# Performance work log

Hardware: AMD Instinct MI355X
Metric: run time of the kernel (lower is better)

The kernel has to match this reference:

```python
import jax, jax.numpy as jnp
import numpy as np
import math

B, S, E, H, F, V, L = 2, 2048, 1024, 16, 4096, 32000, 2
D = E // H
START = 1
EPS = 1e-6


def setup_inputs() -> dict:
    key = jax.random.key(0)
    ks = jax.random.split(key, 16)
    k_emb = 1.0 / math.sqrt(V)
    std = 0.02
    inp = {
        "tokens": jax.random.randint(ks[0], (B, S), 0, V),
        "word_embed": jax.random.normal(ks[1], (V, E), jnp.float32) * k_emb,
        "pos_embed": jax.random.normal(ks[2], (S, E), jnp.float32) * k_emb,
        "unembed_b": jnp.zeros((V,), jnp.float32),
        "kqv_w": jax.random.normal(ks[3], (L, 3 * E, E), jnp.float32) * std,
        "wo_w": jax.random.normal(ks[4], (L, E, E), jnp.float32) * std,
        "up_w": jax.random.normal(ks[5], (L, F, E), jnp.float32) * std,
        "up_b": jnp.zeros((L, F), jnp.float32),
        "down_w": jax.random.normal(ks[6], (L, E, F), jnp.float32) * std,
        "down_b": jnp.zeros((L, E), jnp.float32),
        "ln1_s": jnp.ones((L, E), jnp.float32),
        "ln1_b": jnp.zeros((L, E), jnp.float32),
        "ln2_s": jnp.ones((L, E), jnp.float32),
        "ln2_b": jnp.zeros((L, E), jnp.float32),
    }
    return inp


def _layer_norm(x, scale, bias):
    m = jnp.mean(x, axis=-1, keepdims=True)
    v = jnp.var(x, axis=-1, keepdims=True)  # biased, matches torch LayerNorm
    return (x - m) / jnp.sqrt(v + EPS) * scale + bias


def _causal_block_mask(tokens):
    # block-diagonal segments split at START tokens, plus causal triu
    is_start = tokens == START
    seg = jnp.cumsum(is_start, axis=1)  # [B,S]
    block = seg[:, :, None] != seg[:, None, :]  # [B,S,S]
    triu = jnp.triu(jnp.ones((S, S), bool), k=1)
    return triu[None, :, :] | block  # [B,S,S], True = masked


def _resetting_positions(tokens):
    is_start = tokens == START
    is_start = is_start.at[:, 0].set(True)
    pos = jnp.arange(S)
    start_pos = jnp.where(is_start, pos[None, :], 0)
    last_start = jax.lax.cummax(start_pos, axis=1)
    return pos[None, :] - last_start  # [B,S]


def reference(tokens, word_embed, pos_embed, unembed_b, kqv_w, wo_w,
              up_w, up_b, down_w, down_b, ln1_s, ln1_b, ln2_s, ln2_b):
    mask = _causal_block_mask(tokens)[:, None, :, :]  # [B,1,S,S]
    rel_pos = _resetting_positions(tokens)
    x = word_embed[tokens] + pos_embed[rel_pos]  # [B,S,E]
    scale = 1.0 / math.sqrt(D)

    for l in range(L):
        # attention
        qkv = (x @ kqv_w[l].T).reshape(B, S, 3, H, D)
        k, q, v = qkv[:, :, 0], qkv[:, :, 1], qkv[:, :, 2]  # [B,S,H,D]
        attn = jnp.einsum('bqhd,bkhd->bhqk', q, k) * scale
        attn = jnp.where(mask, -jnp.inf, attn)
        attn = jax.nn.softmax(attn, axis=-1)
        out = jnp.einsum('bhqk,bkhd->bqhd', attn, v).reshape(B, S, E)
        out = out @ wo_w[l].T
        x = _layer_norm(out + x, ln1_s[l], ln1_b[l])
        # FFN
        h = jax.nn.relu(x @ up_w[l].T + up_b[l])
        h = h @ down_w[l].T + down_b[l]
        x = _layer_norm(h + x, ln2_s[l], ln2_b[l])

    # weight-tied unembed
    logits = x @ word_embed.T + unembed_b  # [B,S,V]
    return logits
```

## Files before the change

kernel.cpp:

```cpp
#include <hip/hip_runtime.h>
#include <hip/hip_bf16.h>

#define BB 2
#define SS 2048
#define EE 1024
#define HH 16
#define DD 64
#define FF 4096
#define VV 32000
#define LL 2
#define BS (BB*SS)

#define NEG_HUGE (-3.402823466e+38f)

typedef __attribute__((ext_vector_type(4)))  float  f32x4;
typedef __attribute__((ext_vector_type(16))) float  f32x16;
typedef __attribute__((ext_vector_type(8)))  __bf16 bf16x8;
typedef __attribute__((ext_vector_type(4)))  __bf16 bf16x4;

__device__ inline bf16x8 to_bf8(float4 a, float4 b) {
  bf16x8 r;
  r[0] = (__bf16)a.x; r[1] = (__bf16)a.y; r[2] = (__bf16)a.z; r[3] = (__bf16)a.w;
  r[4] = (__bf16)b.x; r[5] = (__bf16)b.y; r[6] = (__bf16)b.z; r[7] = (__bf16)b.w;
  return r;
}

typedef const unsigned int __attribute__((address_space(1)))* gptr_t;
typedef unsigned int __attribute__((address_space(3)))* lptr_t;
__device__ inline void gload16(const void* g, void* l) {
  __builtin_amdgcn_global_load_lds((gptr_t)g, (lptr_t)l, 16, 0, 0);
}

__global__ __launch_bounds__(1024) void lastart_scan(
    const int* __restrict__ tokens, int* __restrict__ ls) {
  __shared__ int buf[SS];
  const int b = blockIdx.x, t = threadIdx.x;
#pragma unroll
  for (int j = 0; j < 2; ++j) {
    int i = t + j * 1024;
    buf[i] = (i > 0 && tokens[b*SS + i] == 1) ? i : 0;
  }
  __syncthreads();
  for (int off = 1; off < SS; off <<= 1) {
    int i0 = t, i1 = t + 1024;
    int v0 = (i0 >= off) ? max(buf[i0], buf[i0 - off]) : buf[i0];
    int v1 = (i1 >= off) ? max(buf[i1], buf[i1 - off]) : buf[i1];
    __syncthreads();
    buf[i0] = v0; buf[i1] = v1;
    __syncthreads();
  }
#pragma unroll
  for (int j = 0; j < 2; ++j) {
    int i = t + j * 1024;
    ls[b*SS + i] = buf[i];
  }
}

__global__ __launch_bounds__(256) void embed_kernel(
    const int* __restrict__ tokens, const int* __restrict__ ls,
    const float* __restrict__ we, const float* __restrict__ pe,
    float* __restrict__ x, __bf16* __restrict__ xb) {
  int row = blockIdx.x;
  int s = row & (SS - 1);
  int tok = tokens[row];
  int rp = s - ls[row];
  const float4* w4 = (const float4*)(we + (size_t)tok * EE);
  const float4* p4 = (const float4*)(pe + (size_t)rp * EE);
  float4 a = w4[threadIdx.x];
  float4 b = p4[threadIdx.x];
  float4 o; o.x = a.x + b.x; o.y = a.y + b.y; o.z = a.z + b.z; o.w = a.w + b.w;
  ((float4*)(x + (size_t)row * EE))[threadIdx.x] = o;
  bf16x4 ob4;
  ob4[0] = (__bf16)o.x; ob4[1] = (__bf16)o.y; ob4[2] = (__bf16)o.z; ob4[3] = (__bf16)o.w;
  *(bf16x4*)(xb + (size_t)row * EE + threadIdx.x * 4) = ob4;
}

__global__ __launch_bounds__(256) void cvt_bf16_kernel(
    const float* __restrict__ src, __bf16* __restrict__ dst, int n) {
  int i = (blockIdx.x * 256 + threadIdx.x) * 8;
  if (i + 8 > n) return;
  float4 a = *(const float4*)(src + i);
  float4 b = *(const float4*)(src + i + 4);
  *(bf16x8*)(dst + i) = to_bf8(a, b);
}

__device__ inline void stage_half(const __bf16* __restrict__ base,
                                  __bf16* region, int K, int kofs, int t) {
  const int col8 = (t & 3) ^ ((t >> 3) & 3);
  const int csrc = kofs + col8 * 8;
  const int wbase = (t >> 6) * 512;
#pragma unroll
  for (int p = 0; p < 2; ++p)
    gload16(base + (size_t)(p * 128 + (t >> 2)) * K + csrc, region + p * 4096 + wbase);
}

#define SWZ(row) ((c8 ^ (((row) >> 1) & 3)) * 8)

template<bool BIAS, bool RELU, bool OUTBF16>
__global__ __launch_bounds__(512, 2) void gemm_8ph(
    const __bf16* __restrict__ A, const __bf16* __restrict__ W,
    const float* __restrict__ bias, void* __restrict__ Cv,
    int N, int K, int nbx) {
  __shared__ __bf16 lds[2][2][2][8192];
  const int t = threadIdx.x, l = t & 63, w = t >> 6;
  const int nwg = gridDim.x, orig = blockIdx.x;
  const int q = nwg >> 3, r = nwg & 7, xcd = orig & 7, pos = orig >> 3;
  const int wgid = (xcd < r ? xcd*(q+1) : r*(q+1) + (xcd-r)*q) + pos;
  const int m0 = (wgid % nbx) * 256, n0 = (wgid / nbx) * 256;
  const int wm = w >> 2, wn = w & 3;
  const int fr = l & 15, c8 = l >> 4;

  const __bf16* Ab = A + (size_t)m0 * K;
  const __bf16* Wb = W + (size_t)n0 * K;

  f32x4 acc[8][4] = {};
  const int nk = K >> 6;

  stage_half(Ab, &lds[0][0][0][0], K, 0,  t);
  stage_half(Wb, &lds[0][1][0][0], K, 0,  t);
  stage_half(Ab, &lds[0][0][1][0], K, 32, t);
  stage_half(Wb, &lds[0][1][1][0], K, 32, t);
  stage_half(Ab, &lds[1][0][0][0], K, 64, t);
  stage_half(Wb, &lds[1][1][0][0], K, 64, t);
  asm volatile("s_waitcnt vmcnt(4)" ::: "memory");
  __builtin_amdgcn_s_barrier();
  __builtin_amdgcn_sched_barrier(0);

  for (int kt = 0; kt < nk; ++kt) {
    const int c = kt & 1;
    bf16x8 afr[4], bfr[4];
#pragma unroll
    for (int j = 0; j < 4; ++j) {
      const int row = wn*64 + j*16 + fr;
      bfr[j] = *(const bf16x8*)&lds[c][1][0][row*32 + SWZ(row)];
    }
#pragma unroll
    for (int i = 0; i < 4; ++i) {
      const int row = wm*128 + i*16 + fr;
      afr[i] = *(const bf16x8*)&lds[c][0][0][row*32 + SWZ(row)];
    }
    if (kt + 1 < nk) stage_half(Ab, &lds[c^1][0][1][0], K, (kt+1)*64 + 32, t);
    __builtin_amdgcn_s_barrier();
    __builtin_amdgcn_sched_barrier(0);
    __builtin_amdgcn_s_setprio(1);
#pragma unroll
    for (int i = 0; i < 4; ++i)
#pragma unroll
      for (int j = 0; j < 4; ++j)
        acc[i][j] = __builtin_amdgcn_mfma_f32_16x16x32_bf16(afr[i], bfr[j], acc[i][j], 0, 0, 0);
    __builtin_amdgcn_s_setprio(0);
    __builtin_amdgcn_sched_barrier(0);
    __builtin_amdgcn_s_barrier();
    __builtin_amdgcn_sched_barrier(0);
#pragma unroll
    for (int i = 0; i < 4; ++i) {
      const int row = wm*128 + (i+4)*16 + fr;
      afr[i] = *(const bf16x8*)&lds[c][0][0][row*32 + SWZ(row)];
    }
    if (kt + 1 < nk) stage_half(Wb, &lds[c^1][1][1][0], K, (kt+1)*64 + 32, t);
    __builtin_amdgcn_s_barrier();
    __builtin_amdgcn_sched_barrier(0);
    __builtin_amdgcn_s_setprio(1);
#pragma unroll
    for (int i = 0; i < 4; ++i)
#pragma unroll
      for (int j = 0; j < 4; ++j)
        acc[i+4][j] = __builtin_amdgcn_mfma_f32_16x16x32_bf16(afr[i], bfr[j], acc[i+4][j], 0, 0, 0);
    __builtin_amdgcn_s_setprio(0);
    __builtin_amdgcn_sched_barrier(0);
    if (kt < nk - 1) { asm volatile("s_waitcnt vmcnt(8)" ::: "memory"); }
    else             { asm volatile("s_waitcnt vmcnt(0)" ::: "memory"); }
    __builtin_amdgcn_s_barrier();
    __builtin_amdgcn_sched_barrier(0);
#pragma unroll
    for (int j = 0; j < 4; ++j) {
      const int row = wn*64 + j*16 + fr;
      bfr[j] = *(const bf16x8*)&lds[c][1][1][row*32 + SWZ(row)];
    }
#pragma unroll
    for (int i = 0; i < 4; ++i) {
      const int row = wm*128 + i*16 + fr;
      afr[i] = *(const bf16x8*)&lds[c][0][1][row*32 + SWZ(row)];
    }
    if (kt + 2 < nk) stage_half(Ab, &lds[c][0][0][0], K, (kt+2)*64, t);
    __builtin_amdgcn_s_barrier();
    __builtin_amdgcn_sched_barrier(0);
    __builtin_amdgcn_s_setprio(1);
#pragma unroll
    for (int i = 0; i < 4; ++i)
#pragma unroll
      for (int j = 0; j < 4; ++j)
        acc[i][j] = __builtin_amdgcn_mfma_f32_16x16x32_bf16(afr[i], bfr[j], acc[i][j], 0, 0, 0);
    __builtin_amdgcn_s_setprio(0);
    __builtin_amdgcn_sched_barrier(0);
    __builtin_amdgcn_s_barrier();
    __builtin_amdgcn_sched_barrier(0);
#pragma unroll
    for (int i = 0; i < 4; ++i) {
      const int row = wm*128 + (i+4)*16 + fr;
      afr[i] = *(const bf16x8*)&lds[c][0][1][row*32 + SWZ(row)];
    }
    if (kt + 2 < nk) stage_half(Wb, &lds[c][1][0][0], K, (kt+2)*64, t);
    __builtin_amdgcn_s_barrier();
    __builtin_amdgcn_sched_barrier(0);
    __builtin_amdgcn_s_setprio(1);
#pragma unroll
    for (int i = 0; i < 4; ++i)
#pragma unroll
      for (int j = 0; j < 4; ++j)
        acc[i+4][j] = __builtin_amdgcn_mfma_f32_16x16x32_bf16(afr[i], bfr[j], acc[i+4][j], 0, 0, 0);
    __builtin_amdgcn_s_setprio(0);
    __builtin_amdgcn_sched_barrier(0);
    if (kt < nk - 2)       { asm volatile("s_waitcnt vmcnt(8)" ::: "memory"); }
    else if (kt == nk - 2) { asm volatile("s_waitcnt vmcnt(4)" ::: "memory"); }
    __builtin_amdgcn_s_barrier();
    __builtin_amdgcn_sched_barrier(0);
  }

  const int orow = m0 + wm*128 + c8 * 4;
  const int ocol = n0 + wn*64 + fr;
#pragma unroll
  for (int i = 0; i < 8; ++i)
#pragma unroll
    for (int j = 0; j < 4; ++j) {
      const int col = ocol + j * 16;
      const float bv = BIAS ? bias[col] : 0.0f;
#pragma unroll
      for (int rr = 0; rr < 4; ++rr) {
        float v = acc[i][j][rr] + bv;
        if (RELU) v = fmaxf(v, 0.0f);
        if (OUTBF16)
          ((__bf16*)Cv)[(size_t)(orow + i*16 + rr) * N + col] = (__bf16)v;
        else
          ((float*)Cv)[(size_t)(orow + i*16 + rr) * N + col] = v;
      }
    }
}

template<int T, int BM>
__device__ inline void stage2(const __bf16* __restrict__ Ab,
                              const __bf16* __restrict__ Wb,
                              __bf16* la, __bf16* lb, int K, int k0, int t) {
  const int col8 = (t & 3) ^ ((t >> 3) & 3);
  const int cofs = k0 + col8 * 8;
  const int wbase = (t >> 6) * 512;
#pragma unroll
  for (int p = 0; p < (BM * 32) / (T * 8); ++p) {
    const int row = p * (T >> 2) + (t >> 2);
    gload16(Ab + (size_t)row * K + cofs, la + p * T * 8 + wbase);
    gload16(Wb + (size_t)row * K + cofs, lb + p * T * 8 + wbase);
  }
}

template<int RW, int WM, int WN, bool BIAS, bool RELU, bool OUTBF16>
__global__ __launch_bounds__(WM*WN*64, 2) void gemm_deep(
    const __bf16* __restrict__ A, const __bf16* __restrict__ W,
    const float* __restrict__ bias, void* __restrict__ Cv,
    int N, int K, int nbx) {
  constexpr int T  = WM * WN * 64;
  constexpr int BM = WM * RW * 16;
  __shared__ __bf16 lds[4][2][BM * 32];
  const int t = threadIdx.x, l = t & 63, w = t >> 6;
  const int nwg = gridDim.x, orig = blockIdx.x;
  const int q = nwg >> 3, r = nwg & 7, xcd = orig & 7, pos = orig >> 3;
  const int wgid = (xcd < r ? xcd*(q+1) : r*(q+1) + (xcd-r)*q) + pos;
  const int m0 = (wgid % nbx) * BM, n0 = (wgid / nbx) * BM;
  const int wm = w / WN, wn = w % WN;
  const int fr = l & 15, c8 = l >> 4;
  const int slot = (c8 ^ ((fr >> 1) & 3)) * 8;

  const __bf16* Abase = A + (size_t)m0 * K;
  const __bf16* Wbase = W + (size_t)n0 * K;

  f32x4 acc[RW][4] = {};

  const int nk = K >> 5;
  stage2<T,BM>(Abase, Wbase, &lds[0][0][0], &lds[0][1][0], K, 0,  t);
  stage2<T,BM>(Abase, Wbase, &lds[1][0][0], &lds[1][1][0], K, 32, t);
  stage2<T,BM>(Abase, Wbase, &lds[2][0][0], &lds[2][1][0], K, 64, t);

  for (int kt = 0; kt < nk; ++kt) {
    const int cur = kt & 3;
    if (kt + 3 < nk) {
      const int nb = (kt + 3) & 3;
      stage2<T,BM>(Abase, Wbase, &lds[nb][0][0], &lds[nb][1][0], K, (kt+3)*32, t);
      asm volatile("s_waitcnt vmcnt(8)" ::: "memory");
    } else if (kt + 2 < nk) {
      asm volatile("s_waitcnt vmcnt(8)" ::: "memory");
    } else if (kt + 1 < nk) {
      asm volatile("s_waitcnt vmcnt(4)" ::: "memory");
    } else {
      asm volatile("s_waitcnt vmcnt(0)" ::: "memory");
    }
    __builtin_amdgcn_s_barrier();
    __builtin_amdgcn_sched_barrier(0);
    const __bf16* La = &lds[cur][0][0];
    const __bf16* Lb = &lds[cur][1][0];
    bf16x8 bfr[4];
#pragma unroll
    for (int j = 0; j < 4; ++j)
      bfr[j] = *(const bf16x8*)&Lb[(wn*64 + j*16 + fr) * 32 + slot];
    __builtin_amdgcn_s_setprio(1);
#pragma unroll
    for (int i = 0; i < RW; ++i) {
      bf16x8 af = *(const bf16x8*)&La[(wm*(RW*16) + i*16 + fr) * 32 + slot];
#pragma unroll
      for (int j = 0; j < 4; ++j)
        acc[i][j] = __builtin_amdgcn_mfma_f32_16x16x32_bf16(af, bfr[j], acc[i][j], 0, 0, 0);
    }
    __builtin_amdgcn_s_setprio(0);
    __builtin_amdgcn_sched_barrier(0);
    __builtin_amdgcn_s_barrier();
    __builtin_amdgcn_sched_barrier(0);
  }

  const int orow = m0 + wm*(RW*16) + c8 * 4;
  const int ocol = n0 + wn*64 + fr;
#pragma unroll
  for (int i = 0; i < RW; ++i)
#pragma unroll
    for (int j = 0; j < 4; ++j) {
      const int col = ocol + j * 16;
      const float bv = BIAS ? bias[col] : 0.0f;
#pragma unroll
      for (int rr = 0; rr < 4; ++rr) {
        float v = acc[i][j][rr] + bv;
        if (RELU) v = fmaxf(v, 0.0f);
        if (OUTBF16)
          ((__bf16*)Cv)[(size_t)(orow + i*16 + rr) * N + col] = (__bf16)v;
        else
          ((float*)Cv)[(size_t)(orow + i*16 + rr) * N + col] = v;
      }
    }
}

template<bool WBF16, bool BIAS, bool RELU, bool OUTBF16>
__global__ __launch_bounds__(256) void gemm_fast(
    const __bf16* __restrict__ A, const void* __restrict__ Wv,
    const float* __restrict__ bias, void* __restrict__ Cv, int N, int K) {
  __shared__ __bf16 As[128][32];
  __shared__ __bf16 Bs[128][32];
  const int t = threadIdx.x;
  const int m0 = blockIdx.x * 128, n0 = blockIdx.y * 128;
  const int l = t & 63, w = t >> 6;
  const int wm = (w >> 1) * 64, wn = (w & 1) * 64;
  const int fr = l & 15, fk = (l >> 4) * 8;
  const int crow = l >> 2, ccol = (l & 3) * 8;
  const int wrow = t >> 1, wcol = (t & 1) * 16;

  const __bf16* Wb = (const __bf16*)Wv;
  const float*  Wf = (const float*)Wv;

  f32x4 acc[4][4] = {};

  for (int k0 = 0; k0 < K; k0 += 32) {
    float4 wf0, wf1, wf2, wf3;
    if (!WBF16) {
      const float* wp = Wf + (size_t)(n0 + wrow) * K + k0 + wcol;
      wf0 = *(const float4*)(wp);
      wf1 = *(const float4*)(wp + 4);
      wf2 = *(const float4*)(wp + 8);
      wf3 = *(const float4*)(wp + 12);
    }
    __syncthreads();
#pragma unroll
    for (int i = 0; i < 2; ++i) {
      const int c = 2 * w + i;
      gload16(A + (size_t)(m0 + c*16 + crow) * K + k0 + ccol, (__bf16*)As + c*512);
      if (WBF16)
        gload16(Wb + (size_t)(n0 + c*16 + crow) * K + k0 + ccol, (__bf16*)Bs + c*512);
    }
    if (!WBF16) {
      *(bf16x8*)&Bs[wrow][wcol]     = to_bf8(wf0, wf1);
      *(bf16x8*)&Bs[wrow][wcol + 8] = to_bf8(wf2, wf3);
    }
    __syncthreads();
    bf16x8 af[4], bf[4];
#pragma unroll
    for (int i = 0; i < 4; ++i) af[i] = *(const bf16x8*)&As[wm + i*16 + fr][fk];
#pragma unroll
    for (int j = 0; j < 4; ++j) bf[j] = *(const bf16x8*)&Bs[wn + j*16 + fr][fk];
#pragma unroll
    for (int i = 0; i < 4; ++i)
#pragma unroll
      for (int j = 0; j < 4; ++j)
        acc[i][j] = __builtin_amdgcn_mfma_f32_16x16x32_bf16(af[i], bf[j], acc[i][j], 0, 0, 0);
  }

  const int orow = m0 + wm + (l >> 4) * 4;
  const int ocol = n0 + wn + fr;
#pragma unroll
  for (int i = 0; i < 4; ++i)
#pragma unroll
    for (int j = 0; j < 4; ++j) {
      const int col = ocol + j * 16;
      const float bv = BIAS ? bias[col] : 0.0f;
#pragma unroll
      for (int r = 0; r < 4; ++r) {
        float v = acc[i][j][r] + bv;
        if (RELU) v = fmaxf(v, 0.0f);
        if (OUTBF16)
          ((__bf16*)Cv)[(size_t)(orow + i*16 + r) * N + col] = (__bf16)v;
        else
          ((float*)Cv)[(size_t)(orow + i*16 + r) * N + col] = v;
      }
    }
}

__global__ __launch_bounds__(256) void ln_res_kernel(
    const float* __restrict__ y, float* __restrict__ x, __bf16* __restrict__ xb,
    const float* __restrict__ sc, const float* __restrict__ bs) {
  __shared__ float red[8];
  int row = blockIdx.x, t = threadIdx.x;
  const float4* y4 = (const float4*)(y + (size_t)row * EE);
  float4* x4 = (float4*)(x + (size_t)row * EE);
  float4 a = y4[t], c = x4[t];
  float v0 = a.x + c.x, v1 = a.y + c.y, v2 = a.z + c.z, v3 = a.w + c.w;
  float s = v0 + v1 + v2 + v3;
  float q = v0*v0 + v1*v1 + v2*v2 + v3*v3;
#pragma unroll
  for (int off = 32; off; off >>= 1) {
    s += __shfl_xor(s, off);
    q += __shfl_xor(q, off);
  }
  int w = t >> 6;
  if ((t & 63) == 0) { red[w] = s; red[4 + w] = q; }
  __syncthreads();
  s = red[0] + red[1] + red[2] + red[3];
  q = red[4] + red[5] + red[6] + red[7];
  float mean = s * (1.0f / EE);
  float var  = q * (1.0f / EE) - mean * mean;
  float r = 1.0f / sqrtf(var + 1e-6f);
  float4 ss = ((const float4*)sc)[t];
  float4 bb = ((const float4*)bs)[t];
  float4 o;
  o.x = (v0 - mean) * r * ss.x + bb.x;
  o.y = (v1 - mean) * r * ss.y + bb.y;
  o.z = (v2 - mean) * r * ss.z + bb.z;
  o.w = (v3 - mean) * r * ss.w + bb.w;
  x4[t] = o;
  bf16x4 ob4;
  ob4[0] = (__bf16)o.x; ob4[1] = (__bf16)o.y; ob4[2] = (__bf16)o.z; ob4[3] = (__bf16)o.w;
  *(bf16x4*)(xb + (size_t)row * EE + t * 4) = ob4;
}

__global__ __launch_bounds__(256) void attn_mfma(
    const __bf16* __restrict__ qkv, const int* __restrict__ ls,
    __bf16* __restrict__ out) {
  const int qt = 15 - blockIdx.x;
  const int h = blockIdx.y, b = blockIdx.z;
  __shared__ f32x4 lds4[2304];
  char* lds = (char*)lds4;
  __bf16* Ks = (__bf16*)lds;
  __bf16* Vs = (__bf16*)(lds + 9216);
  __shared__ int redmin[4];
  const int t = threadIdx.x, w = t >> 6, l = t & 63;
  __bf16* Pq = (__bf16*)(lds + 18432 + w * 4608);
  const int r = l & 31, hi = l >> 5;
  const int qb = qt * 128, qw = qb + w * 32, qg = qw + r;
  const int Lq = ls[b*SS + qg];

  {
    int mn = Lq;
#pragma unroll
    for (int off = 1; off < 64; off <<= 1) mn = min(mn, __shfl_xor(mn, off));
    if (l == 0) redmin[w] = mn;
  }

  bf16x8 qf[4];
  {
    const __bf16* qrow = qkv + (size_t)(b*SS + qg) * 3*EE + EE + h*DD + 8*hi;
#pragma unroll
    for (int ds = 0; ds < 4; ++ds) qf[ds] = *(const bf16x8*)(qrow + 16*ds);
  }
  __syncthreads();
  const int ktmin = min(min(redmin[0], redmin[1]), min(redmin[2], redmin[3])) >> 6;
  const int ktmax = 2*qt + 1;

  f32x16 oacc[2] = {};
  float m_r = NEG_HUGE, lsum = 0.0f;

  for (int kt = ktmin; kt <= ktmax; ++kt) {
    __syncthreads();
    {
      const int kr = t >> 2, c0 = (t & 3) * 16;
      const __bf16* kg = qkv + (size_t)(b*SS + kt*64 + kr) * 3*EE + h*DD + c0;
      const __bf16* vg = kg + 2*EE;
      bf16x8 k0 = *(const bf16x8*)kg;
      bf16x8 k1 = *(const bf16x8*)(kg + 8);
      bf16x8 v0 = *(const bf16x8*)vg;
      bf16x8 v1 = *(const bf16x8*)(vg + 8);
      *(bf16x8*)&Ks[kr*72 + c0]     = k0;
      *(bf16x8*)&Ks[kr*72 + c0 + 8] = k1;
      const int vc = (kr + 8*(t & 3)) & 63;
#pragma unroll
      for (int j = 0; j < 8; ++j) {
        Vs[(c0 + j)*72 + vc]     = v0[j];
        Vs[(c0 + 8 + j)*72 + vc] = v1[j];
      }
    }
    __syncthreads();

    bool act0 = (kt*64)      <= (qw + 31);
    bool act1 = (kt*64 + 32) <= (qw + 31);
    if (!act0) continue;

    f32x16 st[2];
    st[0] = (f32x16){};
    st[1] = (f32x16){};
#pragma unroll
    for (int ds = 0; ds < 4; ++ds) {
      bf16x8 kf = *(const bf16x8*)&Ks[(r)*72 + 16*ds + 8*hi];
      st[0] = __builtin_amdgcn_mfma_f32_32x32x16_bf16(kf, qf[ds], st[0], 0, 0, 0);
    }
    if (act1) {
#pragma unroll
      for (int ds = 0; ds < 4; ++ds) {
        bf16x8 kf = *(const bf16x8*)&Ks[(32 + r)*72 + 16*ds + 8*hi];
        st[1] = __builtin_amdgcn_mfma_f32_32x32x16_bf16(kf, qf[ds], st[1], 0, 0, 0);
      }
    }

    float tmax = NEG_HUGE;
#pragma unroll
    for (int kt2 = 0; kt2 < 2; ++kt2) {
#pragma unroll
      for (int reg = 0; reg < 16; ++reg) {
        const int key = kt*64 + 32*kt2 + (reg & 3) + 8*(reg >> 2) + 4*hi;
        float s = (kt2 == 0 || act1) ? st[kt2][reg] * 0.125f : NEG_HUGE;
        const bool valid = (key >= Lq) && (key <= qg);
        s = valid ? s : NEG_HUGE;
        st[kt2][reg] = s;
        tmax = fmaxf(tmax, s);
      }
    }
    tmax = fmaxf(tmax, __shfl_xor(tmax, 32));
    const float m_new = fmaxf(m_r, tmax);
    const float alpha = __expf(m_r - m_new);
    m_r = m_new;

    float psum = 0.0f;
#pragma unroll
    for (int kt2 = 0; kt2 < 2; ++kt2) {
#pragma unroll
      for (int g2 = 0; g2 < 4; ++g2) {
        bf16x4 pk;
#pragma unroll
        for (int j = 0; j < 4; ++j) {
          float p = __expf(st[kt2][g2*4 + j] - m_new);
          psum += p;
          pk[j] = (__bf16)p;
        }
        *(bf16x4*)&Pq[r*72 + 32*kt2 + 8*g2 + 4*hi] = pk;
      }
    }
    psum += __shfl_xor(psum, 32);
    lsum = lsum * alpha + psum;
    oacc[0] *= alpha;
    oacc[1] *= alpha;

#pragma unroll
    for (int ks = 0; ks < 4; ++ks) {
      if (kt*64 + 16*ks > qw + 31) continue;
      bf16x8 pf = *(const bf16x8*)&Pq[r*72 + 16*ks + 8*hi];
#pragma unroll
      for (int mt = 0; mt < 2; ++mt) {
        const int d = 32*mt + r;
        const int vcol = (16*ks + 8*hi + 8*((d >> 4) & 3)) & 63;
        bf16x8 vf = *(const bf16x8*)&Vs[d*72 + vcol];
        oacc[mt] = __builtin_amdgcn_mfma_f32_32x32x16_bf16(vf, pf, oacc[mt], 0, 0, 0);
      }
    }
  }

  __syncthreads();
  float* Ot = (float*)(lds + w * 8448);
  const float rinv = 1.0f / lsum;
#pragma unroll
  for (int mt = 0; mt < 2; ++mt)
#pragma unroll
    for (int reg = 0; reg < 16; ++reg) {
      const int d = 32*mt + (reg & 3) + 8*(reg >> 2) + 4*hi;
      Ot[d*33 + r] = oacc[mt][reg] * rinv;
    }
  __syncthreads();
  const int qr0 = l >> 4, dc = (l & 15) * 4;
#pragma unroll
  for (int it = 0; it < 8; ++it) {
    const int qr = qr0 + 4*it;
    bf16x4 ov;
    ov[0] = (__bf16)Ot[(dc+0)*33 + qr];
    ov[1] = (__bf16)Ot[(dc+1)*33 + qr];
    ov[2] = (__bf16)Ot[(dc+2)*33 + qr];
    ov[3] = (__bf16)Ot[(dc+3)*33 + qr];
    *(bf16x4*)(out + (size_t)(b*SS + qw + qr) * EE + h*DD + dc) = ov;
  }
}

extern "C" void kernel_launch(void* const* d_in, const int* in_sizes, int n_in,
                              void* d_out, int out_size, void* d_ws, size_t ws_size,
                              hipStream_t stream) {
  const int*   tokens     = (const int*)  d_in[0];
  const float* word_embed = (const float*)d_in[1];
  const float* pos_embed  = (const float*)d_in[2];
  const float* unembed_b  = (const float*)d_in[3];
  const float* kqv_w      = (const float*)d_in[4];
  const float* wo_w       = (const float*)d_in[5];
  const float* up_w       = (const float*)d_in[6];
  const float* up_b       = (const float*)d_in[7];
  const float* down_w     = (const float*)d_in[8];
  const float* down_b     = (const float*)d_in[9];
  const float* ln1_s      = (const float*)d_in[10];
  const float* ln1_b      = (const float*)d_in[11];
  const float* ln2_s      = (const float*)d_in[12];
  const float* ln2_b      = (const float*)d_in[13];
  float* logits = (float*)d_out;

  char* ob = (char*)d_out;
  __bf16* qkv  = (__bf16*)ob;
  __bf16* t0   = (__bf16*)(ob +  24ull*1024*1024);
  __bf16* hbuf = (__bf16*)(ob +  32ull*1024*1024);
  float*  ybuf = (float*) (ob +  64ull*1024*1024);
  __bf16* wcvt = (__bf16*)(ob +  80ull*1024*1024);
  float*  x    = (float*) (ob + 131ull*1024*1024);
  __bf16* kqvb  = wcvt;
  __bf16* wob   = kqvb + (size_t)LL*3*EE*EE;
  __bf16* upb   = wob  + (size_t)LL*EE*EE;
  __bf16* downb = upb  + (size_t)LL*FF*EE;
  int*    ls   = (int*)d_ws;
  __bf16* xb   = (__bf16*)((char*)d_ws + 65536);
  __bf16* webf = (__bf16*)((char*)d_ws + 65536 + 8ull*1024*1024);
  const bool bigws = ws_size >= (size_t)(65536 + 8ull*1024*1024 + (size_t)VV*EE*2);

  lastart_scan<<<BB, 1024, 0, stream>>>(tokens, ls);
  embed_kernel<<<BS, 256, 0, stream>>>(tokens, ls, word_embed, pos_embed, x, xb);

  cvt_bf16_kernel<<<LL*3*EE*EE/2048, 256, 0, stream>>>(kqv_w,  kqvb,  LL*3*EE*EE);
  cvt_bf16_kernel<<<LL*EE*EE/2048,   256, 0, stream>>>(wo_w,   wob,   LL*EE*EE);
  cvt_bf16_kernel<<<LL*FF*EE/2048,   256, 0, stream>>>(up_w,   upb,   LL*FF*EE);
  cvt_bf16_kernel<<<LL*EE*FF/2048,   256, 0, stream>>>(down_w, downb, LL*EE*FF);
  if (bigws)
    cvt_bf16_kernel<<<VV*EE/2048, 256, 0, stream>>>(word_embed, webf, VV*EE);

  for (int l = 0; l < LL; ++l) {
    gemm_8ph<false,false,true><<<(BS/256)*(3*EE/256), 512, 0, stream>>>(
        xb, kqvb + (size_t)l*3*EE*EE, nullptr, qkv, 3*EE, EE, BS/256);
    attn_mfma<<<dim3(16, HH, BB), 256, 0, stream>>>(qkv, ls, t0);
    gemm_deep<4,2,2,false,false,false><<<(BS/128)*(EE/128), 256, 0, stream>>>(
        t0, wob + (size_t)l*EE*EE, nullptr, ybuf, EE, EE, BS/128);
    ln_res_kernel<<<BS, 256, 0, stream>>>(ybuf, x, xb, ln1_s + l*EE, ln1_b + l*EE);
    gemm_8ph<true,true,true><<<(BS/256)*(FF/256), 512, 0, stream>>>(
        xb, upb + (size_t)l*FF*EE, up_b + (size_t)l*FF, hbuf, FF, EE, BS/256);
    gemm_deep<4,2,2,true,false,false><<<(BS/128)*(EE/128), 256, 0, stream>>>(
        hbuf, downb + (size_t)l*EE*FF, down_b + (size_t)l*EE, ybuf, EE, FF, BS/128);
    ln_res_kernel<<<BS, 256, 0, stream>>>(ybuf, x, xb, ln2_s + l*EE, ln2_b + l*EE);
  }

  if (bigws)
    gemm_8ph<true,false,false><<<(BS/256)*(VV/256), 512, 0, stream>>>(
        xb, webf, unembed_b, logits, VV, EE, BS/256);
  else
    gemm_fast<false,true,false,false><<<dim3(BS/128, VV/128), 256, 0, stream>>>(
        xb, word_embed, unembed_b, logits, VV, EE);
}
```

Baseline: 983.0 us.

## Make unembed GEMM workgroups persist over several M tiles with a continuous pipeline

Measured after the change: 915.2 us. -6.9%, faster.

```diff
diff --git a/kernel.cpp b/kernel.cpp
--- a/kernel.cpp
+++ b/kernel.cpp
@@ -84,62 +84,67 @@
   *(bf16x8*)(dst + i) = to_bf8(a, b);
 }
 
-__device__ inline void stage_half(const __bf16* __restrict__ base,
-                                  __bf16* region, int K, int kofs, int t) {
-  const int col8 = (t & 3) ^ ((t >> 3) & 3);
-  const int csrc = kofs + col8 * 8;
-  const int wbase = (t >> 6) * 512;
+__device__ inline void stage_half8(const __bf16* __restrict__ base,
+                                   __bf16* region, int K, int kofs,
+                                   int col8, int srow, int sdst) {
 #pragma unroll
   for (int p = 0; p < 2; ++p)
-    gload16(base + (size_t)(p * 128 + (t >> 2)) * K + csrc, region + p * 4096 + wbase);
-}
-
-#define SWZ(row) ((c8 ^ (((row) >> 1) & 3)) * 8)
-
-template<bool BIAS, bool RELU, bool OUTBF16>
+    gload16(base + (size_t)(p * 128 + srow) * K + kofs + col8,
+            region + p * 4096 + sdst);
+}
+
+template<int NMT, bool BIAS, bool RELU, bool OUTBF16>
 __global__ __launch_bounds__(512, 2) void gemm_8ph(
     const __bf16* __restrict__ A, const __bf16* __restrict__ W,
     const float* __restrict__ bias, void* __restrict__ Cv,
-    int N, int K, int nbx) {
-  __shared__ __bf16 lds[2][2][2][8192];
+    int N, int K, int nmg) {
+  __shared__ __bf16 lds[8][8192];
   const int t = threadIdx.x, l = t & 63, w = t >> 6;
   const int nwg = gridDim.x, orig = blockIdx.x;
   const int q = nwg >> 3, r = nwg & 7, xcd = orig & 7, pos = orig >> 3;
   const int wgid = (xcd < r ? xcd*(q+1) : r*(q+1) + (xcd-r)*q) + pos;
-  const int m0 = (wgid % nbx) * 256, n0 = (wgid / nbx) * 256;
+  const int mgrp = wgid % nmg, n0 = (wgid / nmg) * 256;
   const int wm = w >> 2, wn = w & 3;
   const int fr = l & 15, c8 = l >> 4;
-
-  const __bf16* Ab = A + (size_t)m0 * K;
+  const int swz = (c8 ^ ((fr >> 1) & 3)) * 8;
+  const int roA = (wm*128 + fr) * 32 + swz;
+  const int roB = (wn*64  + fr) * 32 + swz;
+  const int col8 = ((t & 3) ^ ((t >> 3) & 3)) * 8;
+  const int srow = t >> 2;
+  const int sdst = (t >> 6) * 512;
+
   const __bf16* Wb = W + (size_t)n0 * K;
+  const int ng = NMT * 16;
+
+  float bv[4];
+#pragma unroll
+  for (int j = 0; j < 4; ++j) bv[j] = BIAS ? bias[n0 + wn*64 + fr + j*16] : 0.0f;
 
   f32x4 acc[8][4] = {};
-  const int nk = K >> 6;
-
-  stage_half(Ab, &lds[0][0][0][0], K, 0,  t);
-  stage_half(Wb, &lds[0][1][0][0], K, 0,  t);
-  stage_half(Ab, &lds[0][0][1][0], K, 32, t);
-  stage_half(Wb, &lds[0][1][1][0], K, 32, t);
-  stage_half(Ab, &lds[1][0][0][0], K, 64, t);
-  stage_half(Wb, &lds[1][1][0][0], K, 64, t);
+
+#define ABASE(g2) (A + (size_t)(mgrp*NMT + ((g2) >> 4)) * 256 * K)
+#define KOFS(g2)  (((g2) & 15) * 64)
+
+  stage_half8(ABASE(0), &lds[0][0], K, 0,  col8, srow, sdst);
+  stage_half8(Wb,       &lds[2][0], K, 0,  col8, srow, sdst);
+  stage_half8(ABASE(0), &lds[1][0], K, 32, col8, srow, sdst);
+  stage_half8(Wb,       &lds[3][0], K, 32, col8, srow, sdst);
+  stage_half8(ABASE(1), &lds[4][0], K, 64, col8, srow, sdst);
+  stage_half8(Wb,       &lds[6][0], K, 64, col8, srow, sdst);
   asm volatile("s_waitcnt vmcnt(4)" ::: "memory");
   __builtin_amdgcn_s_barrier();
   __builtin_amdgcn_sched_barrier(0);
 
-  for (int kt = 0; kt < nk; ++kt) {
-    const int c = kt & 1;
+  for (int g = 0; g < ng; ++g) {
+    const int c = g & 1;
+    const int rA = c*4, rB = c*4 + 2;
     bf16x8 afr[4], bfr[4];
 #pragma unroll
-    for (int j = 0; j < 4; ++j) {
-      const int row = wn*64 + j*16 + fr;
-      bfr[j] = *(const bf16x8*)&lds[c][1][0][row*32 + SWZ(row)];
-    }
-#pragma unroll
-    for (int i = 0; i < 4; ++i) {
-      const int row = wm*128 + i*16 + fr;
-      afr[i] = *(const bf16x8*)&lds[c][0][0][row*32 + SWZ(row)];
-    }
-    if (kt + 1 < nk) stage_half(Ab, &lds[c^1][0][1][0], K, (kt+1)*64 + 32, t);
+    for (int j = 0; j < 4; ++j) bfr[j] = *(const bf16x8*)&lds[rB][roB + j*512];
+#pragma unroll
+    for (int i = 0; i < 4; ++i) afr[i] = *(const bf16x8*)&lds[rA][roA + i*512];
+    if (g + 1 < ng)
+      stage_half8(ABASE(g+1), &lds[(c^1)*4 + 1][0], K, KOFS(g+1) + 32, col8, srow, sdst);
     __builtin_amdgcn_s_barrier();
     __builtin_amdgcn_sched_barrier(0);
     __builtin_amdgcn_s_setprio(1);
@@ -153,11 +158,9 @@
     __builtin_amdgcn_s_barrier();
     __builtin_amdgcn_sched_barrier(0);
 #pragma unroll
-    for (int i = 0; i < 4; ++i) {
-      const int row = wm*128 + (i+4)*16 + fr;
-      afr[i] = *(const bf16x8*)&lds[c][0][0][row*32 + SWZ(row)];
-    }
-    if (kt + 1 < nk) stage_half(Wb, &lds[c^1][1][1][0], K, (kt+1)*64 + 32, t);
+    for (int i = 0; i < 4; ++i) afr[i] = *(const bf16x8*)&lds[rA][roA + (i+4)*512];
+    if (g + 1 < ng)
+      stage_half8(Wb, &lds[(c^1)*4 + 3][0], K, KOFS(g+1) + 32, col8, srow, sdst);
     __builtin_amdgcn_s_barrier();
     __builtin_amdgcn_sched_barrier(0);
     __builtin_amdgcn_s_setprio(1);
@@ -168,21 +171,16 @@
         acc[i+4][j] = __builtin_amdgcn_mfma_f32_16x16x32_bf16(afr[i], bfr[j], acc[i+4][j], 0, 0, 0);
     __builtin_amdgcn_s_setprio(0);
     __builtin_amdgcn_sched_barrier(0);
-    if (kt < nk - 1) { asm volatile("s_waitcnt vmcnt(8)" ::: "memory"); }
-    else             { asm volatile("s_waitcnt vmcnt(0)" ::: "memory"); }
-    __builtin_amdgcn_s_barrier();
-    __builtin_amdgcn_sched_barrier(0);
-#pragma unroll
-    for (int j = 0; j < 4; ++j) {
-      const int row = wn*64 + j*16 + fr;
-      bfr[j] = *(const bf16x8*)&lds[c][1][1][row*32 + SWZ(row)];
-    }
-#pragma unroll
-    for (int i = 0; i < 4; ++i) {
-      const int row = wm*128 + i*16 + fr;
-      afr[i] = *(const bf16x8*)&lds[c][0][1][row*32 + SWZ(row)];
-    }
-    if (kt + 2 < nk) stage_half(Ab, &lds[c][0][0][0], K, (kt+2)*64, t);
+    if (g < ng - 1) { asm volatile("s_waitcnt vmcnt(8)" ::: "memory"); }
+    else            { asm volatile("s_waitcnt vmcnt(0)" ::: "memory"); }
+    __builtin_amdgcn_s_barrier();
+    __builtin_amdgcn_sched_barrier(0);
+#pragma unroll
+    for (int j = 0; j < 4; ++j) bfr[j] = *(const bf16x8*)&lds[rB + 1][roB + j*512];
+#pragma unroll
+    for (int i = 0; i < 4; ++i) afr[i] = *(const bf16x8*)&lds[rA + 1][roA + i*512];
+    if (g + 2 < ng)
+      stage_half8(ABASE(g+2), &lds[c*4][0], K, KOFS(g+2), col8, srow, sdst);
     __builtin_amdgcn_s_barrier();
     __builtin_amdgcn_sched_barrier(0);
     __builtin_amdgcn_s_setprio(1);
@@ -196,11 +194,9 @@
     __builtin_amdgcn_s_barrier();
     __builtin_amdgcn_sched_barrier(0);
 #pragma unroll
-    for (int i = 0; i < 4; ++i) {
-      const int row = wm*128 + (i+4)*16 + fr;
-      afr[i] = *(const bf16x8*)&lds[c][0][1][row*32 + SWZ(row)];
-    }
-    if (kt + 2 < nk) stage_half(Wb, &lds[c][1][0][0], K, (kt+2)*64, t);
+    for (int i = 0; i < 4; ++i) afr[i] = *(const bf16x8*)&lds[rA + 1][roA + (i+4)*512];
+    if (g + 2 < ng)
+      stage_half8(Wb, &lds[c*4 + 2][0], K, KOFS(g+2), col8, srow, sdst);
     __builtin_amdgcn_s_barrier();
     __builtin_amdgcn_sched_barrier(0);
     __builtin_amdgcn_s_setprio(1);
@@ -211,30 +207,32 @@
         acc[i+4][j] = __builtin_amdgcn_mfma_f32_16x16x32_bf16(afr[i], bfr[j], acc[i+4][j], 0, 0, 0);
     __builtin_amdgcn_s_setprio(0);
     __builtin_amdgcn_sched_barrier(0);
-    if (kt < nk - 2)       { asm volatile("s_waitcnt vmcnt(8)" ::: "memory"); }
-    else if (kt == nk - 2) { asm volatile("s_waitcnt vmcnt(4)" ::: "memory"); }
-    __builtin_amdgcn_s_barrier();
-    __builtin_amdgcn_sched_barrier(0);
-  }
-
-  const int orow = m0 + wm*128 + c8 * 4;
-  const int ocol = n0 + wn*64 + fr;
-#pragma unroll
-  for (int i = 0; i < 8; ++i)
-#pragma unroll
-    for (int j = 0; j < 4; ++j) {
-      const int col = ocol + j * 16;
-      const float bv = BIAS ? bias[col] : 0.0f;
-#pragma unroll
-      for (int rr = 0; rr < 4; ++rr) {
-        float v = acc[i][j][rr] + bv;
-        if (RELU) v = fmaxf(v, 0.0f);
-        if (OUTBF16)
-          ((__bf16*)Cv)[(size_t)(orow + i*16 + rr) * N + col] = (__bf16)v;
-        else
-          ((float*)Cv)[(size_t)(orow + i*16 + rr) * N + col] = v;
-      }
-    }
+    if (g < ng - 2)       { asm volatile("s_waitcnt vmcnt(8)" ::: "memory"); }
+    else if (g == ng - 2) { asm volatile("s_waitcnt vmcnt(4)" ::: "memory"); }
+    __builtin_amdgcn_s_barrier();
+    __builtin_amdgcn_sched_barrier(0);
+    if ((g & 15) == 15) {
+      const int orow = (mgrp*NMT + (g >> 4)) * 256 + wm*128 + c8 * 4;
+      const int ocol = n0 + wn*64 + fr;
+#pragma unroll
+      for (int i = 0; i < 8; ++i)
+#pragma unroll
+        for (int j = 0; j < 4; ++j) {
+#pragma unroll
+          for (int rr = 0; rr < 4; ++rr) {
+            float v = acc[i][j][rr] + bv[j];
+            if (RELU) v = fmaxf(v, 0.0f);
+            if (OUTBF16)
+              ((__bf16*)Cv)[(size_t)(orow + i*16 + rr) * N + ocol + j*16] = (__bf16)v;
+            else
+              ((float*)Cv)[(size_t)(orow + i*16 + rr) * N + ocol + j*16] = v;
+          }
+          acc[i][j] = (f32x4){};
+        }
+    }
+  }
+#undef ABASE
+#undef KOFS
 }
 
 template<int T, int BM>
@@ -643,23 +641,24 @@
     cvt_bf16_kernel<<<VV*EE/2048, 256, 0, stream>>>(word_embed, webf, VV*EE);
 
   for (int l = 0; l < LL; ++l) {
-    gemm_8ph<false,false,true><<<(BS/256)*(3*EE/256), 512, 0, stream>>>(
+    gemm_8ph<1,false,false,true><<<(BS/256)*(3*EE/256), 512, 0, stream>>>(
         xb, kqvb + (size_t)l*3*EE*EE, nullptr, qkv, 3*EE, EE, BS/256);
     attn_mfma<<<dim3(16, HH, BB), 256, 0, stream>>>(qkv, ls, t0);
     gemm_deep<4,2,2,false,false,false><<<(BS/128)*(EE/128), 256, 0, stream>>>(
         t0, wob + (size_t)l*EE*EE, nullptr, ybuf, EE, EE, BS/128);
     ln_res_kernel<<<BS, 256, 0, stream>>>(ybuf, x, xb, ln1_s + l*EE, ln1_b + l*EE);
-    gemm_8ph<true,true,true><<<(BS/256)*(FF/256), 512, 0, stream>>>(
+    gemm_8ph<1,true,true,true><<<(BS/256)*(FF/256), 512, 0, stream>>>(
         xb, upb + (size_t)l*FF*EE, up_b + (size_t)l*FF, hbuf, FF, EE, BS/256);
     gemm_deep<4,2,2,true,false,false><<<(BS/128)*(EE/128), 256, 0, stream>>>(
         hbuf, downb + (size_t)l*EE*FF, down_b + (size_t)l*EE, ybuf, EE, FF, BS/128);
     ln_res_kernel<<<BS, 256, 0, stream>>>(ybuf, x, xb, ln2_s + l*EE, ln2_b + l*EE);
   }
 
-  if (bigws)
-    gemm_8ph<true,false,false><<<(BS/256)*(VV/256), 512, 0, stream>>>(
-        xb, webf, unembed_b, logits, VV, EE, BS/256);
-  else
+  if (bigws) {
+    gemm_8ph<8,true,false,false><<<(VV/256)*2, 512, 0, stream>>>(
+        xb, webf, unembed_b, logits, VV, EE, 2);
+  } else {
     gemm_fast<false,true,false,false><<<dim3(BS/128, VV/128), 256, 0, stream>>>(
         xb, word_embed, unembed_b, logits, VV, EE);
-}
+  }
+}
```
